# Kernel optimization log

Hardware: AMD Instinct MI355X
Metric: run time of the kernel (lower is better)

## Reference

```python
import jax, jax.numpy as jnp
import numpy as np

N_NODES = 100000
N_EDGES = 600000
DIMS = [128, 64, 32, 2]


def gcn_conv(x, edge_index, W, b, n_nodes):
    """PyG GCNConv (eval mode): symmetric-normalized aggregation with self-loops.
    out = D^{-1/2} (A + I) D^{-1/2} (x W) + b
    """
    h = x @ W  # [N, out] -- transform first (cheaper when out < in)
    src = jnp.concatenate([edge_index[0], jnp.arange(n_nodes)])  # add self-loops
    dst = jnp.concatenate([edge_index[1], jnp.arange(n_nodes)])
    deg = jax.ops.segment_sum(jnp.ones_like(dst, dtype=h.dtype), dst,
                              num_segments=n_nodes)  # in-degree incl. self-loop
    dinv = jax.lax.rsqrt(deg)
    norm = dinv[src] * dinv[dst]  # [E+N]
    msg = norm[:, None] * h[src]  # gather + scale
    out = jax.ops.segment_sum(msg, dst, num_segments=n_nodes)  # scatter-add
    return out + b


def setup_inputs() -> dict:
    key = jax.random.key(0)
    ks = jax.random.split(key, 8)
    x = jax.random.normal(ks[0], (N_NODES, DIMS[0]), dtype=jnp.float32)
    edge_index = jax.random.randint(ks[1], (2, N_EDGES), 0, N_NODES, dtype=jnp.int64)
    inp = {"x": x, "edge_index": edge_index}
    for i in range(3):
        fan_in, fan_out = DIMS[i], DIMS[i + 1]
        s = 1.0 / np.sqrt(fan_in)
        inp[f"W{i+1}"] = jax.random.uniform(ks[2 + 2 * i], (fan_in, fan_out),
                                            minval=-s, maxval=s, dtype=jnp.float32)
        inp[f"b{i+1}"] = jnp.zeros((fan_out,), dtype=jnp.float32)
    return inp


def reference(x, edge_index, W1, b1, W2, b2, W3, b3):
    # 3 stacked GCNConv layers with ReLU; dropout is identity in eval mode.
    n = x.shape[0]
    x = jax.nn.relu(gcn_conv(x, edge_index, W1, b1, n))
    x = jax.nn.relu(gcn_conv(x, edge_index, W2, b2, n))
    x = jax.nn.relu(gcn_conv(x, edge_index, W3, b3, n))
    return x
```

## Files before the change

kernel.cpp:

```cpp
#include <hip/hip_runtime.h>
#include <math.h>


#define FULL_GRID 2048
#define PARTS 8

typedef const __attribute__((address_space(1))) void* gas_ptr;
typedef __attribute__((address_space(3))) void* las_ptr;
typedef __attribute__((ext_vector_type(8))) short bf16x8;
typedef __attribute__((ext_vector_type(4))) float f32x4;

__device__ __forceinline__ void gld16(const void* g, void* l) {
  __builtin_amdgcn_global_load_lds((gas_ptr)g, (las_ptr)l, 16, 0, 0);
}

__device__ __forceinline__ unsigned short f2bf(float f) {
  unsigned int u = __float_as_uint(f);
  u += 0x7FFF + ((u >> 16) & 1);
  return (unsigned short)(u >> 16);
}
__device__ __forceinline__ float bf2f(unsigned short h) {
  return __uint_as_float(((unsigned int)h) << 16);
}

__global__ __launch_bounds__(256) void k_init(int* __restrict__ p, int n4,
                                              const unsigned int* __restrict__ words,
                                              int* __restrict__ flag,
                                              const float* __restrict__ W1,
                                              const float* __restrict__ W2,
                                              short* __restrict__ Wh1,
                                              short* __restrict__ Wl1,
                                              short* __restrict__ Wh2,
                                              short* __restrict__ Wl2) {
  if (blockIdx.x == 128) {
    __shared__ int sm[256];
    int cnt = 0;
    #pragma unroll
    for (int j = 0; j < 8; ++j) {
      int idx = (threadIdx.x * 8 + j) * 2 + 1;
      cnt += (words[idx] == 0u) ? 1 : 0;
    }
    sm[threadIdx.x] = cnt;
    __syncthreads();
    for (int off = 128; off > 0; off >>= 1) {
      if (threadIdx.x < off) sm[threadIdx.x] += sm[threadIdx.x + off];
      __syncthreads();
    }
    if (threadIdx.x == 0) flag[0] = (sm[0] > 1024) ? 1 : 0;
    return;
  }
  if (blockIdx.x > 128) {
    const int t = (blockIdx.x - 129) * 256 + threadIdx.x;
    const int stride = 32 * 256;
    for (int q = t; q < 4 * 4 * 64 * 8; q += stride) {
      const int e = q & 7, lane = (q >> 3) & 63, nt = (q >> 9) & 3, kt = q >> 11;
      const int k = kt * 32 + (lane >> 4) * 8 + e;
      const int nn = nt * 16 + (lane & 15);
      const float f = W1[k * 64 + nn];
      const unsigned short h = f2bf(f);
      Wh1[q] = (short)h;
      Wl1[q] = (short)f2bf(f - bf2f(h));
    }
    for (int q = t; q < 2 * 2 * 64 * 8; q += stride) {
      const int e = q & 7, lane = (q >> 3) & 63, nt = (q >> 9) & 1, kt = q >> 10;
      const int k = kt * 32 + (lane >> 4) * 8 + e;
      const int nn = nt * 16 + (lane & 15);
      const float f = W2[k * 32 + nn];
      const unsigned short h = f2bf(f);
      Wh2[q] = (short)h;
      Wl2[q] = (short)f2bf(f - bf2f(h));
    }
    return;
  }
  int i = blockIdx.x * blockDim.x + threadIdx.x;
  const int stride = 128 * blockDim.x;
  int4* p4 = (int4*)p;
  for (; i < n4; i += stride) p4[i] = make_int4(0, 0, 0, 0);
}

__global__ __launch_bounds__(256) void k_normalize(const void* __restrict__ eraw,
                                                   int E,
                                                   const int* __restrict__ flag,
                                                   int* __restrict__ srcn,
                                                   int* __restrict__ dstn) {
  const int is64 = flag[0];
  int i = blockIdx.x * blockDim.x + threadIdx.x;
  const int stride = gridDim.x * blockDim.x;
  if (is64) {
    const long long* e = (const long long*)eraw;
    for (; i < E; i += stride) {
      srcn[i] = (int)e[i];
      dstn[i] = (int)e[(long long)E + i];
    }
  } else {
    const int* e = (const int*)eraw;
    for (; i < E; i += stride) {
      srcn[i] = e[i];
      dstn[i] = e[E + i];
    }
  }
}

__global__ __launch_bounds__(256) void k_hist(const int* __restrict__ dstn, int E,
                                              int N, int* __restrict__ counts) {
  const int part = blockIdx.x & (PARTS - 1);
  const int lo = (int)((long long)N * part / PARTS);
  const int hi = (int)((long long)N * (part + 1) / PARTS);
  int i = (blockIdx.x >> 3) * blockDim.x + threadIdx.x;
  const int stride = (gridDim.x >> 3) * blockDim.x;
  for (; i < E; i += stride) {
    const int d = dstn[i];
    if (d >= lo && d < hi) atomicAdd(&counts[d], 1);
  }
}

__global__ __launch_bounds__(1024) void k_scan1(const int* __restrict__ counts,
                                                int* __restrict__ scanned,
                                                int* __restrict__ partials, int n) {
  __shared__ int sm[1024];
  const int i = blockIdx.x * 1024 + threadIdx.x;
  const int v = (i < n) ? counts[i] : 0;
  sm[threadIdx.x] = v;
  __syncthreads();
  for (int off = 1; off < 1024; off <<= 1) {
    int t = sm[threadIdx.x];
    int u = (threadIdx.x >= off) ? sm[threadIdx.x - off] : 0;
    __syncthreads();
    sm[threadIdx.x] = t + u;
    __syncthreads();
  }
  const int inc = sm[threadIdx.x];
  if (i < n) scanned[i] = inc - v;
  if (threadIdx.x == 1023) partials[blockIdx.x] = inc;
}

__global__ __launch_bounds__(256) void k_scan3(const int* __restrict__ scanned,
                                               const int* __restrict__ partials,
                                               int nb,
                                               const int* __restrict__ counts,
                                               int* __restrict__ offsets,
                                               int* __restrict__ cursor,
                                               float* __restrict__ dinv, int n) {
  __shared__ int ps[1024];
  for (int t = threadIdx.x; t < nb; t += 256) ps[t] = partials[t];
  __syncthreads();
  if (threadIdx.x == 0) {
    int run = 0;
    for (int b = 0; b < nb; ++b) { const int v = ps[b]; ps[b] = run; run += v; }
  }
  __syncthreads();
  int i = blockIdx.x * blockDim.x + threadIdx.x;
  const int stride = gridDim.x * blockDim.x;
  for (; i < n; i += stride) {
    const int o = scanned[i] + ps[i >> 10];
    offsets[i] = o;
    cursor[i] = o;
    dinv[i] = rsqrtf((float)counts[i] + 1.0f);
  }
}

__global__ __launch_bounds__(256) void k_fill(const int* __restrict__ srcn,
                                              const int* __restrict__ dstn, int E,
                                              int N, int* __restrict__ cursor,
                                              int* __restrict__ elist) {
  const int part = blockIdx.x & (PARTS - 1);
  const int lo = (int)((long long)N * part / PARTS);
  const int hi = (int)((long long)N * (part + 1) / PARTS);
  int i = (blockIdx.x >> 3) * blockDim.x + threadIdx.x;
  const int stride = (gridDim.x >> 3) * blockDim.x;
  for (; i < E; i += stride) {
    const int d = dstn[i];
    if (d >= lo && d < hi) elist[atomicAdd(&cursor[d], 1)] = srcn[i];
  }
}

template <int F_IN, int F_OUT>
__global__ __launch_bounds__(256) void k_transform_mfma(
    const float* __restrict__ X, const short* __restrict__ Wh,
    const short* __restrict__ Wl, const float* __restrict__ dinv,
    float* __restrict__ H, int n) {
  constexpr int KT = F_IN / 32;
  constexpr int NT = F_OUT / 16;
  constexpr int K4f = F_IN / 4;
  constexpr int SLOTS = F_IN / 8;
  constexpr int TILE_M = 64;
  constexpr int WFRAG = KT * NT * 64 * 8;
  static_assert((WFRAG * 2) % 1024 == 0, "W segs");

  __shared__ __align__(16) unsigned short Xh[TILE_M * F_IN];
  __shared__ __align__(16) unsigned short Xl[TILE_M * F_IN];
  __shared__ __align__(16) unsigned short Whs[WFRAG];
  __shared__ __align__(16) unsigned short Wls[WFRAG];

  const int tid = threadIdx.x;
  const int lane = tid & 63;
  const int wid = tid >> 6;
  const long long base = (long long)blockIdx.x * TILE_M;

  constexpr int WSEGS = WFRAG * 2 / 1024;
  for (int seg = wid; seg < WSEGS; seg += 4) {
    gld16((const char*)Wh + seg * 1024 + lane * 16, (char*)Whs + seg * 1024);
    gld16((const char*)Wl + seg * 1024 + lane * 16, (char*)Wls + seg * 1024);
  }

  const float4* __restrict__ X4 = (const float4*)X;
  for (int g = tid; g < TILE_M * K4f; g += 256) {
    const int row = g / K4f, c4 = g % K4f;
    float4 v = make_float4(0.f, 0.f, 0.f, 0.f);
    if (base + row < n) v = X4[(base + row) * K4f + c4];
    ushort4 hv, lv;
    hv.x = f2bf(v.x); lv.x = f2bf(v.x - bf2f(hv.x));
    hv.y = f2bf(v.y); lv.y = f2bf(v.y - bf2f(hv.y));
    hv.z = f2bf(v.z); lv.z = f2bf(v.z - bf2f(hv.z));
    hv.w = f2bf(v.w); lv.w = f2bf(v.w - bf2f(hv.w));
    const int slot = (c4 >> 1) ^ (row & (SLOTS - 1));
    const int boff = row * (F_IN * 2) + slot * 16 + (c4 & 1) * 8;
    *(ushort4*)((char*)Xh + boff) = hv;
    *(ushort4*)((char*)Xl + boff) = lv;
  }
  __syncthreads();

  const int arow = lane & 15;
  const int kg = lane >> 4;
  const int lrow = wid * 16 + arow;

  f32x4 acc[NT];
  #pragma unroll
  for (int t = 0; t < NT; ++t) {
    f32x4 z = {0.f, 0.f, 0.f, 0.f};
    acc[t] = z;
  }

  #pragma unroll
  for (int kt = 0; kt < KT; ++kt) {
    const int slot = (kt * 4 + kg) ^ (lrow & (SLOTS - 1));
    const int aoff = lrow * (F_IN * 2) + slot * 16;
    const bf16x8 ah = *(const bf16x8*)((const char*)Xh + aoff);
    const bf16x8 al = *(const bf16x8*)((const char*)Xl + aoff);
    #pragma unroll
    for (int nt = 0; nt < NT; ++nt) {
      const int woff = ((kt * NT + nt) * 64 + lane) * 8;
      const bf16x8 bh = *(const bf16x8*)&Whs[woff];
      const bf16x8 bl = *(const bf16x8*)&Wls[woff];
      acc[nt] = __builtin_amdgcn_mfma_f32_16x16x32_bf16(ah, bh, acc[nt], 0, 0, 0);
      acc[nt] = __builtin_amdgcn_mfma_f32_16x16x32_bf16(ah, bl, acc[nt], 0, 0, 0);
      acc[nt] = __builtin_amdgcn_mfma_f32_16x16x32_bf16(al, bh, acc[nt], 0, 0, 0);
    }
  }

  #pragma unroll
  for (int r = 0; r < 4; ++r) {
    const long long row = base + wid * 16 + kg * 4 + r;
    if (row < n) {
      const float di = dinv[row];
      #pragma unroll
      for (int nt = 0; nt < NT; ++nt)
        H[row * F_OUT + nt * 16 + arow] = di * acc[nt][r];
    }
  }
}

template <int F, bool RELU_OUT, bool FUSE_W3>
__global__ __launch_bounds__(256) void k_agg_vec2(const float* __restrict__ HS,
                                                  const float* __restrict__ dinv,
                                                  const int* __restrict__ offsets,
                                                  const int* __restrict__ counts,
                                                  const int* __restrict__ elist,
                                                  const float* __restrict__ bias,
                                                  const float* __restrict__ W3,
                                                  float* __restrict__ out, int n) {
  constexpr int LPE = F / 4;
  constexpr int EPW = 64 / LPE;
  const int lane = threadIdx.x & 63;
  const int wv = (blockIdx.x * (blockDim.x >> 6)) + (threadIdx.x >> 6);
  const int nwaves = gridDim.x * (blockDim.x >> 6);
  const int g = lane / LPE;
  const int fl = lane % LPE;
  const float4 bf = *(const float4*)&bias[fl * 4];

  float w3a0 = 0.f, w3a1 = 0.f, w3a2 = 0.f, w3a3 = 0.f;
  float w3b0 = 0.f, w3b1 = 0.f, w3b2 = 0.f, w3b3 = 0.f;
  if (FUSE_W3) {
    w3a0 = W3[(fl * 4 + 0) * 2 + 0]; w3b0 = W3[(fl * 4 + 0) * 2 + 1];
    w3a1 = W3[(fl * 4 + 1) * 2 + 0]; w3b1 = W3[(fl * 4 + 1) * 2 + 1];
    w3a2 = W3[(fl * 4 + 2) * 2 + 0]; w3b2 = W3[(fl * 4 + 2) * 2 + 1];
    w3a3 = W3[(fl * 4 + 3) * 2 + 0]; w3b3 = W3[(fl * 4 + 3) * 2 + 1];
  }

  for (long long dA = wv; dA < n; dA += 2ll * nwaves) {
    const long long dB = dA + nwaves;
    const bool hasB = dB < n;
    const float diA = dinv[dA];
    const float diB = hasB ? dinv[dB] : 0.f;
    const int stA = offsets[dA];
    const int cntA = counts[dA];
    const int stB = hasB ? offsets[dB] : 0;
    const int cntB = hasB ? counts[dB] : 0;
    float4 accA = make_float4(0.f, 0.f, 0.f, 0.f);
    float4 accB = make_float4(0.f, 0.f, 0.f, 0.f);
    if (g == 0) accA = *(const float4*)&HS[dA * F + fl * 4];
    if (g == 1 && hasB) accB = *(const float4*)&HS[dB * F + fl * 4];

    const int jmax = cntA > cntB ? cntA : cntB;
    const int cA = cntA > 0 ? cntA - 1 : 0;
    const int cB = cntB > 0 ? cntB - 1 : 0;
    for (int j = 0; j < jmax; j += 2 * EPW) {
      const int e0 = j + g;
      const int e1 = j + EPW + g;
      const int iA0 = elist[stA + (e0 < cntA ? e0 : cA)];
      const int iA1 = elist[stA + (e1 < cntA ? e1 : cA)];
      const int iB0 = elist[stB + (e0 < cntB ? e0 : cB)];
      const int iB1 = elist[stB + (e1 < cntB ? e1 : cB)];
      const float4 vA0 = *(const float4*)&HS[(long long)iA0 * F + fl * 4];
      const float4 vA1 = *(const float4*)&HS[(long long)iA1 * F + fl * 4];
      const float4 vB0 = *(const float4*)&HS[(long long)iB0 * F + fl * 4];
      const float4 vB1 = *(const float4*)&HS[(long long)iB1 * F + fl * 4];
      if (e0 < cntA) {
        accA.x += vA0.x; accA.y += vA0.y; accA.z += vA0.z; accA.w += vA0.w;
      }
      if (e1 < cntA) {
        accA.x += vA1.x; accA.y += vA1.y; accA.z += vA1.z; accA.w += vA1.w;
      }
      if (e0 < cntB) {
        accB.x += vB0.x; accB.y += vB0.y; accB.z += vB0.z; accB.w += vB0.w;
      }
      if (e1 < cntB) {
        accB.x += vB1.x; accB.y += vB1.y; accB.z += vB1.z; accB.w += vB1.w;
      }
    }
    #pragma unroll
    for (int m = LPE; m < 64; m <<= 1) {
      accA.x += __shfl_xor(accA.x, m, 64);
      accA.y += __shfl_xor(accA.y, m, 64);
      accA.z += __shfl_xor(accA.z, m, 64);
      accA.w += __shfl_xor(accA.w, m, 64);
      accB.x += __shfl_xor(accB.x, m, 64);
      accB.y += __shfl_xor(accB.y, m, 64);
      accB.z += __shfl_xor(accB.z, m, 64);
      accB.w += __shfl_xor(accB.w, m, 64);
    }
    float4 rA, rB;
    rA.x = fmaf(diA, accA.x, bf.x); rA.y = fmaf(diA, accA.y, bf.y);
    rA.z = fmaf(diA, accA.z, bf.z); rA.w = fmaf(diA, accA.w, bf.w);
    rB.x = fmaf(diB, accB.x, bf.x); rB.y = fmaf(diB, accB.y, bf.y);
    rB.z = fmaf(diB, accB.z, bf.z); rB.w = fmaf(diB, accB.w, bf.w);
    if (RELU_OUT) {
      rA.x = fmaxf(rA.x, 0.f); rA.y = fmaxf(rA.y, 0.f);
      rA.z = fmaxf(rA.z, 0.f); rA.w = fmaxf(rA.w, 0.f);
      rB.x = fmaxf(rB.x, 0.f); rB.y = fmaxf(rB.y, 0.f);
      rB.z = fmaxf(rB.z, 0.f); rB.w = fmaxf(rB.w, 0.f);
    }
    if (!FUSE_W3) {
      if (g == 0) *(float4*)&out[dA * F + fl * 4] = rA;
      if (g == 1 && hasB) *(float4*)&out[dB * F + fl * 4] = rB;
    } else {
      float tA0 = rA.x * w3a0 + rA.y * w3a1 + rA.z * w3a2 + rA.w * w3a3;
      float tA1 = rA.x * w3b0 + rA.y * w3b1 + rA.z * w3b2 + rA.w * w3b3;
      float tB0 = rB.x * w3a0 + rB.y * w3a1 + rB.z * w3a2 + rB.w * w3a3;
      float tB1 = rB.x * w3b0 + rB.y * w3b1 + rB.z * w3b2 + rB.w * w3b3;
      #pragma unroll
      for (int m = 1; m < LPE; m <<= 1) {
        tA0 += __shfl_xor(tA0, m, 64);
        tA1 += __shfl_xor(tA1, m, 64);
        tB0 += __shfl_xor(tB0, m, 64);
        tB1 += __shfl_xor(tB1, m, 64);
      }
      if (lane == 0) {
        out[dA * 2 + 0] = diA * tA0;
        out[dA * 2 + 1] = diA * tA1;
      }
      if (lane == LPE && hasB) {
        out[dB * 2 + 0] = diB * tB0;
        out[dB * 2 + 1] = diB * tB1;
      }
    }
  }
}

template <int F, bool RELU_OUT>
__global__ __launch_bounds__(256) void k_aggregate(const float* __restrict__ HS,
                                                   const float* __restrict__ dinv,
                                                   const int* __restrict__ offsets,
                                                   const int* __restrict__ counts,
                                                   const int* __restrict__ elist,
                                                   const float* __restrict__ bias,
                                                   float* __restrict__ out, int n) {
  const int f = threadIdx.x % F;
  const int grp = threadIdx.x / F;
  constexpr int GRPS = 256 / F;
  const float bf = bias[f];

  for (long long d = (long long)blockIdx.x * GRPS + grp; d < n;
       d += (long long)gridDim.x * GRPS) {
    const float di = dinv[d];
    float acc = HS[d * F + f];
    const int start = offsets[d];
    const int cnt = counts[d];
    for (int j = 0; j < cnt; j += 8) {
      int idx[8];
      float v[8];
      #pragma unroll
      for (int t = 0; t < 8; ++t) {
        const int jj = (j + t < cnt) ? (j + t) : j;
        idx[t] = elist[start + jj];
      }
      #pragma unroll
      for (int t = 0; t < 8; ++t) v[t] = HS[(long long)idx[t] * F + f];
      #pragma unroll
      for (int t = 0; t < 8; ++t) acc += (j + t < cnt) ? v[t] : 0.f;
    }
    float r = fmaf(di, acc, bf);
    if (RELU_OUT) r = fmaxf(r, 0.f);
    out[d * F + f] = r;
  }
}

extern "C" void kernel_launch(void* const* d_in, const int* in_sizes, int n_in,
                              void* d_out, int out_size, void* d_ws, size_t ws_size,
                              hipStream_t stream) {
  const float* x = (const float*)d_in[0];
  const void* eraw = d_in[1];
  const float* W1 = (const float*)d_in[2];
  const float* b1 = (const float*)d_in[3];
  const float* W2 = (const float*)d_in[4];
  const float* b2 = (const float*)d_in[5];
  const float* W3 = (const float*)d_in[6];
  const float* b3 = (const float*)d_in[7];
  float* out = (float*)d_out;

  const int N = in_sizes[0] / 128;
  const int E = in_sizes[1] / 2;

  char* ws = (char*)d_ws;
  size_t off = 0;
  auto alloc = [&](size_t bytes) -> char* {
    char* p = ws + off;
    off = (off + bytes + 255) & ~(size_t)255;
    return p;
  };
  int*   flag     = (int*)alloc(256);
  int*   counts   = (int*)alloc((size_t)N * 4 + 16);
  int*   scanned  = (int*)alloc((size_t)N * 4);
  int*   partials = (int*)alloc(1024 * 4);
  int*   offsets  = (int*)alloc((size_t)N * 4);
  int*   cursor   = (int*)alloc((size_t)N * 4);
  int*   srcn     = (int*)alloc((size_t)E * 4);
  int*   dstn     = (int*)alloc((size_t)E * 4);
  int*   elist    = (int*)alloc((size_t)E * 4);
  float* dinv     = (float*)alloc((size_t)N * 4);
  short* Wh1      = (short*)alloc(4 * 4 * 64 * 8 * 2);
  short* Wl1      = (short*)alloc(4 * 4 * 64 * 8 * 2);
  short* Wh2      = (short*)alloc(2 * 2 * 64 * 8 * 2);
  short* Wl2      = (short*)alloc(2 * 2 * 64 * 8 * 2);
  float* hbuf     = (float*)alloc((size_t)N * 64 * 4);
  float* obuf     = (float*)alloc((size_t)N * 64 * 4);
  float* h2buf    = (float*)alloc((size_t)N * 32 * 4);
  (void)ws_size; (void)n_in; (void)out_size;

  k_init<<<161, 256, 0, stream>>>(counts, (N + 3) / 4, (const unsigned int*)eraw,
                                  flag, W1, W2, Wh1, Wl1, Wh2, Wl2);
  k_normalize<<<1024, 256, 0, stream>>>(eraw, E, flag, srcn, dstn);
  k_hist<<<FULL_GRID, 256, 0, stream>>>(dstn, E, N, counts);
  const int NB = (N + 1023) >> 10;
  k_scan1<<<NB, 1024, 0, stream>>>(counts, scanned, partials, N);
  k_scan3<<<(N + 255) / 256, 256, 0, stream>>>(scanned, partials, NB, counts,
                                               offsets, cursor, dinv, N);
  k_fill<<<FULL_GRID, 256, 0, stream>>>(srcn, dstn, E, N, cursor, elist);

  k_transform_mfma<128, 64><<<(N + 63) / 64, 256, 0, stream>>>(
      x, Wh1, Wl1, dinv, hbuf, N);
  k_agg_vec2<64, true, false><<<FULL_GRID, 256, 0, stream>>>(
      hbuf, dinv, offsets, counts, elist, b1, nullptr, obuf, N);

  k_transform_mfma<64, 32><<<(N + 63) / 64, 256, 0, stream>>>(
      obuf, Wh2, Wl2, dinv, h2buf, N);
  k_agg_vec2<32, true, true><<<FULL_GRID, 256, 0, stream>>>(
      h2buf, dinv, offsets, counts, elist, b2, W3, hbuf, N);

  k_aggregate<2, true><<<(N + 127) / 128, 256, 0, stream>>>(
      hbuf, dinv, offsets, counts, elist, b3, out, N);
}
```

Measured before the change: 171.1 us.

## Fuse layer-1 aggregation with layer-2 MFMA transform and merge dtype detection into init

Adds a kernel that gathers and sums neighbour rows for layer 1 per 64-node tile, applies bias, ReLU and a bf16 hi/lo split into swizzled LDS, then runs the layer-2 MFMA transform in the same block. This removes the 100000x64 intermediate buffer write and read plus one kernel launch. Separately, edge-index dtype detection and int64-to-int32 normalization are folded into k_init, so each normalization block votes on a smaller sample and the separate flag buffer and kernel go away. The fused aggregation uses a fixed per-block node tiling instead of grid-stride waves, which may hurt load balance on high-degree nodes.

New measurement: 194.3 us. 1.14x slower.

```diff
diff --git a/kernel.cpp b/kernel.cpp
--- a/kernel.cpp
+++ b/kernel.cpp
@@ -24,33 +24,25 @@
 }
 
 __global__ __launch_bounds__(256) void k_init(int* __restrict__ p, int n4,
-                                              const unsigned int* __restrict__ words,
-                                              int* __restrict__ flag,
+                                              const void* __restrict__ eraw, int E,
+                                              int* __restrict__ srcn,
+                                              int* __restrict__ dstn,
                                               const float* __restrict__ W1,
                                               const float* __restrict__ W2,
                                               short* __restrict__ Wh1,
                                               short* __restrict__ Wl1,
                                               short* __restrict__ Wh2,
                                               short* __restrict__ Wl2) {
-  if (blockIdx.x == 128) {
-    __shared__ int sm[256];
-    int cnt = 0;
-    #pragma unroll
-    for (int j = 0; j < 8; ++j) {
-      int idx = (threadIdx.x * 8 + j) * 2 + 1;
-      cnt += (words[idx] == 0u) ? 1 : 0;
-    }
-    sm[threadIdx.x] = cnt;
-    __syncthreads();
-    for (int off = 128; off > 0; off >>= 1) {
-      if (threadIdx.x < off) sm[threadIdx.x] += sm[threadIdx.x + off];
-      __syncthreads();
-    }
-    if (threadIdx.x == 0) flag[0] = (sm[0] > 1024) ? 1 : 0;
+  const int b = blockIdx.x;
+  if (b < 128) {
+    int i = b * blockDim.x + threadIdx.x;
+    const int stride = 128 * blockDim.x;
+    int4* p4 = (int4*)p;
+    for (; i < n4; i += stride) p4[i] = make_int4(0, 0, 0, 0);
     return;
   }
-  if (blockIdx.x > 128) {
-    const int t = (blockIdx.x - 129) * 256 + threadIdx.x;
+  if (b < 160) {
+    const int t = (b - 128) * 256 + threadIdx.x;
     const int stride = 32 * 256;
     for (int q = t; q < 4 * 4 * 64 * 8; q += stride) {
       const int e = q & 7, lane = (q >> 3) & 63, nt = (q >> 9) & 3, kt = q >> 11;
@@ -72,20 +64,18 @@
     }
     return;
   }
-  int i = blockIdx.x * blockDim.x + threadIdx.x;
-  const int stride = 128 * blockDim.x;
-  int4* p4 = (int4*)p;
-  for (; i < n4; i += stride) p4[i] = make_int4(0, 0, 0, 0);
-}
-
-__global__ __launch_bounds__(256) void k_normalize(const void* __restrict__ eraw,
-                                                   int E,
-                                                   const int* __restrict__ flag,
-                                                   int* __restrict__ srcn,
-                                                   int* __restrict__ dstn) {
-  const int is64 = flag[0];
-  int i = blockIdx.x * blockDim.x + threadIdx.x;
-  const int stride = gridDim.x * blockDim.x;
+  __shared__ int sm[256];
+  const unsigned int* words = (const unsigned int*)eraw;
+  sm[threadIdx.x] = (words[threadIdx.x * 2 + 1] == 0u) ? 1 : 0;
+  __syncthreads();
+  for (int off = 128; off > 0; off >>= 1) {
+    if (threadIdx.x < off) sm[threadIdx.x] += sm[threadIdx.x + off];
+    __syncthreads();
+  }
+  const int is64 = sm[0] > 128;
+  const int nb = b - 160;
+  int i = nb * 256 + threadIdx.x;
+  const int stride = 1024 * 256;
   if (is64) {
     const long long* e = (const long long*)eraw;
     for (; i < E; i += stride) {
@@ -256,6 +246,118 @@
       #pragma unroll
       for (int nt = 0; nt < NT; ++nt)
         H[row * F_OUT + nt * 16 + arow] = di * acc[nt][r];
+    }
+  }
+}
+
+__global__ __launch_bounds__(256) void k_agg1_t2(
+    const float* __restrict__ HS1, const float* __restrict__ dinv,
+    const int* __restrict__ offsets, const int* __restrict__ counts,
+    const int* __restrict__ elist, const float* __restrict__ b1,
+    const short* __restrict__ Wh, const short* __restrict__ Wl,
+    float* __restrict__ H2, int n) {
+  constexpr int WFRAG = 2 * 2 * 64 * 8;
+  __shared__ __align__(16) unsigned short Xh[64 * 64];
+  __shared__ __align__(16) unsigned short Xl[64 * 64];
+  __shared__ __align__(16) unsigned short Whs[WFRAG];
+  __shared__ __align__(16) unsigned short Wls[WFRAG];
+
+  const int tid = threadIdx.x;
+  const int lane = tid & 63;
+  const int wid = tid >> 6;
+  const long long base = (long long)blockIdx.x * 64;
+
+  gld16((const char*)Wh + wid * 1024 + lane * 16, (char*)Whs + wid * 1024);
+  gld16((const char*)Wl + wid * 1024 + lane * 16, (char*)Wls + wid * 1024);
+
+  const int g = lane >> 4;
+  const int fl = lane & 15;
+  const float4 bf = *(const float4*)&b1[fl * 4];
+
+  for (int t = 0; t < 16; ++t) {
+    const int rl = wid * 16 + t;
+    const long long d = base + rl;
+    float4 r = make_float4(0.f, 0.f, 0.f, 0.f);
+    if (d < n) {
+      const float di = dinv[d];
+      float4 acc = make_float4(0.f, 0.f, 0.f, 0.f);
+      if (g == 0) acc = *(const float4*)&HS1[d * 64 + fl * 4];
+      const int start = offsets[d];
+      const int cnt = counts[d];
+      const int cl = cnt > 0 ? cnt - 1 : 0;
+      for (int j = 0; j < cnt; j += 8) {
+        const int e0 = j + g;
+        const int e1 = j + 4 + g;
+        const int i0 = elist[start + (e0 < cnt ? e0 : cl)];
+        const int i1 = elist[start + (e1 < cnt ? e1 : cl)];
+        const float4 v0 = *(const float4*)&HS1[(long long)i0 * 64 + fl * 4];
+        const float4 v1 = *(const float4*)&HS1[(long long)i1 * 64 + fl * 4];
+        if (e0 < cnt) {
+          acc.x += v0.x; acc.y += v0.y; acc.z += v0.z; acc.w += v0.w;
+        }
+        if (e1 < cnt) {
+          acc.x += v1.x; acc.y += v1.y; acc.z += v1.z; acc.w += v1.w;
+        }
+      }
+      #pragma unroll
+      for (int m = 16; m < 64; m <<= 1) {
+        acc.x += __shfl_xor(acc.x, m, 64);
+        acc.y += __shfl_xor(acc.y, m, 64);
+        acc.z += __shfl_xor(acc.z, m, 64);
+        acc.w += __shfl_xor(acc.w, m, 64);
+      }
+      r.x = fmaxf(fmaf(di, acc.x, bf.x), 0.f);
+      r.y = fmaxf(fmaf(di, acc.y, bf.y), 0.f);
+      r.z = fmaxf(fmaf(di, acc.z, bf.z), 0.f);
+      r.w = fmaxf(fmaf(di, acc.w, bf.w), 0.f);
+    }
+    if (g == 0) {
+      ushort4 hv, lv;
+      hv.x = f2bf(r.x); lv.x = f2bf(r.x - bf2f(hv.x));
+      hv.y = f2bf(r.y); lv.y = f2bf(r.y - bf2f(hv.y));
+      hv.z = f2bf(r.z); lv.z = f2bf(r.z - bf2f(hv.z));
+      hv.w = f2bf(r.w); lv.w = f2bf(r.w - bf2f(hv.w));
+      const int boff = rl * 128 + (((fl >> 1) ^ (rl & 7)) * 16) + (fl & 1) * 8;
+      *(ushort4*)((char*)Xh + boff) = hv;
+      *(ushort4*)((char*)Xl + boff) = lv;
+    }
+  }
+  __syncthreads();
+
+  const int arow = lane & 15;
+  const int kg = lane >> 4;
+  const int lrow = wid * 16 + arow;
+
+  f32x4 acc[2];
+  #pragma unroll
+  for (int t = 0; t < 2; ++t) {
+    f32x4 z = {0.f, 0.f, 0.f, 0.f};
+    acc[t] = z;
+  }
+
+  #pragma unroll
+  for (int kt = 0; kt < 2; ++kt) {
+    const int slot = (kt * 4 + kg) ^ (lrow & 7);
+    const bf16x8 ah = *(const bf16x8*)&Xh[lrow * 64 + slot * 8];
+    const bf16x8 al = *(const bf16x8*)&Xl[lrow * 64 + slot * 8];
+    #pragma unroll
+    for (int nt = 0; nt < 2; ++nt) {
+      const int woff = ((kt * 2 + nt) * 64 + lane) * 8;
+      const bf16x8 bh = *(const bf16x8*)&Whs[woff];
+      const bf16x8 bl = *(const bf16x8*)&Wls[woff];
+      acc[nt] = __builtin_amdgcn_mfma_f32_16x16x32_bf16(ah, bh, acc[nt], 0, 0, 0);
+      acc[nt] = __builtin_amdgcn_mfma_f32_16x16x32_bf16(ah, bl, acc[nt], 0, 0, 0);
+      acc[nt] = __builtin_amdgcn_mfma_f32_16x16x32_bf16(al, bh, acc[nt], 0, 0, 0);
+    }
+  }
+
+  #pragma unroll
+  for (int r = 0; r < 4; ++r) {
+    const long long row = base + wid * 16 + kg * 4 + r;
+    if (row < n) {
+      const float di = dinv[row];
+      H2[row * 32 + 0 * 16 + arow] = di * acc[0][r];
+      H2[row * 32 + 1 * 16 + arow] = di * acc[1][r];
     }
   }
 }
@@ -438,7 +540,6 @@
     off = (off + bytes + 255) & ~(size_t)255;
     return p;
   };
-  int*   flag     = (int*)alloc(256);
   int*   counts   = (int*)alloc((size_t)N * 4 + 16);
   int*   scanned  = (int*)alloc((size_t)N * 4);
   int*   partials = (int*)alloc(1024 * 4);
@@ -453,13 +554,11 @@
   short* Wh2      = (short*)alloc(2 * 2 * 64 * 8 * 2);
   short* Wl2      = (short*)alloc(2 * 2 * 64 * 8 * 2);
   float* hbuf     = (float*)alloc((size_t)N * 64 * 4);
-  float* obuf     = (float*)alloc((size_t)N * 64 * 4);
   float* h2buf    = (float*)alloc((size_t)N * 32 * 4);
   (void)ws_size; (void)n_in; (void)out_size;
 
-  k_init<<<161, 256, 0, stream>>>(counts, (N + 3) / 4, (const unsigned int*)eraw,
-                                  flag, W1, W2, Wh1, Wl1, Wh2, Wl2);
-  k_normalize<<<1024, 256, 0, stream>>>(eraw, E, flag, srcn, dstn);
+  k_init<<<1184, 256, 0, stream>>>(counts, (N + 3) / 4, eraw, E, srcn, dstn,
+                                   W1, W2, Wh1, Wl1, Wh2, Wl2);
   k_hist<<<FULL_GRID, 256, 0, stream>>>(dstn, E, N, counts);
   const int NB = (N + 1023) >> 10;
   k_scan1<<<NB, 1024, 0, stream>>>(counts, scanned, partials, N);
@@ -469,14 +568,10 @@
 
   k_transform_mfma<128, 64><<<(N + 63) / 64, 256, 0, stream>>>(
       x, Wh1, Wl1, dinv, hbuf, N);
-  k_agg_vec2<64, true, false><<<FULL_GRID, 256, 0, stream>>>(
-      hbuf, dinv, offsets, counts, elist, b1, nullptr, obuf, N);
-
-  k_transform_mfma<64, 32><<<(N + 63) / 64, 256, 0, stream>>>(
-      obuf, Wh2, Wl2, dinv, h2buf, N);
+  k_agg1_t2<<<(N + 63) / 64, 256, 0, stream>>>(
+      hbuf, dinv, offsets, counts, elist, b1, Wh2, Wl2, h2buf, N);
   k_agg_vec2<32, true, true><<<FULL_GRID, 256, 0, stream>>>(
       h2buf, dinv, offsets, counts, elist, b2, W3, hbuf, N);
-
   k_aggregate<2, true><<<(N + 127) / 128, 256, 0, stream>>>(
       hbuf, dinv, offsets, counts, elist, b3, out, N);
 }
```
